# Kernel optimization log

Hardware: AMD Instinct MI355X
Metric: run time of the kernel (lower is better)

The kernel has to match this reference:

```python
import jax, jax.numpy as jnp
import numpy as np
from jax import lax

NPRE = 900        # num_proposal_pre (hardcoded in module)
NPOST = 64        # num_proposal init arg
MAXV = 8          # max vertices of intersection of two convex quads
NMS_THRESH = 0.85
BN_EPS = 1e-5


def boxes3d_to_bev(b):
    # b: (N,7) = (x,y,z,h,w,l,ry) -> BEV rotated box (x1,y1,x2,y2,ry) on x-z plane
    cu, cv = b[:, 0], b[:, 2]
    half_l, half_w = b[:, 5] * 0.5, b[:, 4] * 0.5
    return jnp.stack([cu - half_l, cv - half_w, cu + half_l, cv + half_w, b[:, 6]], axis=-1)


def rect_corners(bev):
    # bev: (N,5) -> (N,4,2) CCW corners of rotated rect
    cx = (bev[:, 0] + bev[:, 2]) * 0.5
    cy = (bev[:, 1] + bev[:, 3]) * 0.5
    hx = (bev[:, 2] - bev[:, 0]) * 0.5
    hy = (bev[:, 3] - bev[:, 1]) * 0.5
    c, s = jnp.cos(bev[:, 4]), jnp.sin(bev[:, 4])
    lx = jnp.stack([-hx, hx, hx, -hx], -1)   # (N,4)
    ly = jnp.stack([-hy, -hy, hy, hy], -1)
    X = cx[:, None] + c[:, None] * lx - s[:, None] * ly
    Y = cy[:, None] + s[:, None] * lx + c[:, None] * ly
    return jnp.stack([X, Y], -1)


def _clip(poly, cnt, a, b):
    # Sutherland-Hodgman clip of poly (MAXV,2) with cnt valid verts by half-plane
    # left of directed edge a->b (clip quad is CCW).
    n = b - a
    def side(p):
        return n[0] * (p[1] - a[1]) - n[1] * (p[0] - a[0])
    out = jnp.zeros_like(poly)
    ocnt = jnp.int32(0)
    for i in range(MAXV):
        valid = i < cnt
        cur = poly[i]
        nxt = poly[jnp.where(i + 1 < cnt, i + 1, 0)]
        dc, dn = side(cur), side(nxt)
        in_c, in_n = dc >= 0, dn >= 0
        e1 = valid & in_c
        out = jnp.where(e1, out.at[ocnt].set(cur), out)
        ocnt = ocnt + e1.astype(jnp.int32)
        e2 = valid & (in_c != in_n)
        denom = dc - dn
        t = dc / jnp.where(denom == 0, 1.0, denom)
        ip = cur + t * (nxt - cur)
        out = jnp.where(e2, out.at[ocnt].set(ip), out)
        ocnt = ocnt + e2.astype(jnp.int32)
    return out, ocnt


def _pair_inter(ca, cb):
    # intersection area of two convex quads given CCW corners (4,2)
    poly = jnp.concatenate([ca, jnp.zeros((MAXV - 4, 2), ca.dtype)], 0)
    cnt = jnp.int32(4)
    for k in range(4):
        poly, cnt = _clip(poly, cnt, cb[k], cb[(k + 1) % 4])
    s = jnp.float32(0.0)
    for i in range(MAXV):
        valid = (i < cnt) & (cnt >= 3)
        j = jnp.where(i + 1 < cnt, i + 1, 0)
        s = s + jnp.where(valid, poly[i, 0] * poly[j, 1] - poly[j, 0] * poly[i, 1], 0.0)
    return jnp.abs(s) * 0.5


def pairwise_iou(corners, areas):
    # row-blocked to keep memory small: lax.map over rows, vmap over cols
    def row(args):
        ci, ai = args
        inter = jax.vmap(lambda cj: _pair_inter(ci, cj))(corners)
        return inter / jnp.maximum(ai + areas - inter, 1e-8)
    return lax.map(row, (corners, areas))


def nms_keep(iou):
    N = iou.shape[0]
    idx = jnp.arange(N)
    def body(i, keep):
        sup = keep[i] & (iou[i] > NMS_THRESH) & (idx > i)
        return keep & (~sup)
    return lax.fori_loop(0, N, body, jnp.ones((N,), bool))


def _forward(search_xyz, search_feature, estimation_cla, template_box,
             W1, b1, gamma, beta, run_mean, run_var, W2, b2):
    B, N = search_xyz.shape[0], search_xyz.shape[1]
    # reg head: conv1d(256->128,k1) + BN(eval) + ReLU + dropout(eval=id) + conv1d(128->4,k1)
    h = jnp.einsum('oi,bin->bon', W1, search_feature) + b1[None, :, None]
    inv = gamma / jnp.sqrt(run_var + BN_EPS)
    h = h * inv[None, :, None] + (beta - run_mean * inv)[None, :, None]
    h = jax.nn.relu(h)
    offset = jnp.einsum('oi,bin->bon', W2, h) + b2[None, :, None]  # (B,4,N)
    offset = jnp.transpose(offset, (0, 2, 1))                       # (B,N,4)
    vote_xyz = search_xyz + offset[..., 0:3]
    tmpl = jnp.broadcast_to(template_box, (B, N, 7))
    proposals = jnp.concatenate([vote_xyz, tmpl[..., 3:6], offset[..., 3:4]], -1)  # (B,N,7)
    scores = jax.nn.sigmoid(estimation_cla[..., 0])  # (B,N)

    def per_batch(sc, pr):
        order = jnp.argsort(-sc)
        s = sc[order[:NPRE]]
        p = pr[order[:NPRE]]
        bev = boxes3d_to_bev(p)
        corners = rect_corners(bev)
        areas = (bev[:, 2] - bev[:, 0]) * (bev[:, 3] - bev[:, 1])
        iou = pairwise_iou(lax.stop_gradient(corners), lax.stop_gradient(areas))
        keep = nms_keep(iou)
        rank = jnp.cumsum(keep.astype(jnp.int32)) - 1
        tgt = jnp.where(keep & (rank < NPOST), rank, NPOST)  # NPOST = dummy slot
        out_b = jnp.zeros((NPOST + 1, 7), p.dtype).at[tgt].set(p)[:NPOST]
        out_s = jnp.zeros((NPOST + 1,), s.dtype).at[tgt].set(s)[:NPOST]
        return out_b, out_s

    ret_bbox3d, ret_scores = jax.vmap(per_batch)(scores, proposals)
    center_xyzs = ret_bbox3d[..., 0:3]
    prop_out = jnp.take(proposals, jnp.array([0, 1, 2, 6]), axis=-1)
    return ret_bbox3d, ret_scores, prop_out, center_xyzs


def setup_inputs():
    key = jax.random.key(0)
    ks = jax.random.split(key, 8)
    B, N, C, H = 8, 16384, 256, 128
    search_xyz = jax.random.normal(ks[0], (B, N, 3), jnp.float32) * 2.0
    search_feature = jax.random.normal(ks[1], (B, C, N), jnp.float32)
    estimation_cla = jax.random.normal(ks[2], (B, N, 1), jnp.float32)
    center = jax.random.normal(ks[3], (B, 1, 3), jnp.float32)
    dims = jax.random.uniform(ks[4], (B, 1, 3), jnp.float32, 1.0, 3.0)
    ry = jax.random.uniform(ks[5], (B, 1, 1), jnp.float32, -np.pi, np.pi)
    template_box = jnp.concatenate([center, dims, ry], -1)
    W1 = jax.random.normal(ks[6], (H, C), jnp.float32) * (1.0 / np.sqrt(C))
    b1 = jnp.zeros((H,), jnp.float32)
    gamma = jnp.ones((H,), jnp.float32)
    beta = jnp.zeros((H,), jnp.float32)
    run_mean = jnp.zeros((H,), jnp.float32)
    run_var = jnp.ones((H,), jnp.float32)
    W2 = jax.random.normal(ks[7], (4, H), jnp.float32) * (1.0 / np.sqrt(H))
    b2 = jnp.zeros((4,), jnp.float32)
    return dict(search_xyz=search_xyz, search_feature=search_feature,
                estimation_cla=estimation_cla, template_box=template_box,
                W1=W1, b1=b1, gamma=gamma, beta=beta,
                run_mean=run_mean, run_var=run_var, W2=W2, b2=b2)


def reference(search_xyz, search_feature, estimation_cla, template_box,
              W1, b1, gamma, beta, run_mean, run_var, W2, b2):
    return _forward(search_xyz, search_feature, estimation_cla, template_box,
                    W1, b1, gamma, beta, run_mean, run_var, W2, b2)
```

## Files before the change

### kernel.cpp

```cpp
#include <hip/hip_runtime.h>
#include <cmath>

#define NTOT 16384
#define NBATCH 8
#define NPRE 900
#define NPOST 64

__global__ __launch_bounds__(256) void mlp_kernel(
    const float* __restrict__ feat, const float* __restrict__ xyz,
    const float* __restrict__ W1, const float* __restrict__ b1,
    const float* __restrict__ gamma, const float* __restrict__ beta,
    const float* __restrict__ rmean, const float* __restrict__ rvar,
    const float* __restrict__ W2, const float* __restrict__ b2,
    float* __restrict__ prop) {
  __shared__ float As[64][128];
  __shared__ float Bs[64][128];
  const int b  = blockIdx.y;
  const int n0 = blockIdx.x * 128;
  const int tid = threadIdx.x;
  const int tr = tid >> 4, tc = tid & 15;
  const float* fb = feat + (size_t)b * 256 * NTOT;

  float acc[8][8];
#pragma unroll
  for (int r = 0; r < 8; ++r)
#pragma unroll
    for (int c = 0; c < 8; ++c) acc[r][c] = 0.f;

  for (int kt = 0; kt < 4; ++kt) {
    {
      const int m = tid & 127, qh = tid >> 7;
#pragma unroll
      for (int p = 0; p < 8; ++p) {
        const int q = qh + p * 2;
        const float4 w = *(const float4*)(W1 + (size_t)m * 256 + kt * 64 + q * 4);
        As[q * 4 + 0][m] = w.x; As[q * 4 + 1][m] = w.y;
        As[q * 4 + 2][m] = w.z; As[q * 4 + 3][m] = w.w;
      }
      const int qq = tid & 31, r0 = tid >> 5;
#pragma unroll
      for (int p = 0; p < 8; ++p) {
        const int k = r0 + p * 8;
        *(float4*)(&Bs[k][qq * 4]) =
            *(const float4*)(fb + (size_t)(kt * 64 + k) * NTOT + n0 + qq * 4);
      }
    }
    __syncthreads();
#pragma unroll 8
    for (int k = 0; k < 64; ++k) {
      float a[8], bb[8];
      *(float4*)&a[0]  = *(const float4*)&As[k][tr * 8];
      *(float4*)&a[4]  = *(const float4*)&As[k][tr * 8 + 4];
      *(float4*)&bb[0] = *(const float4*)&Bs[k][tc * 4];
      *(float4*)&bb[4] = *(const float4*)&Bs[k][64 + tc * 4];
#pragma unroll
      for (int r = 0; r < 8; ++r)
#pragma unroll
        for (int c = 0; c < 8; ++c) acc[r][c] = fmaf(a[r], bb[c], acc[r][c]);
    }
    __syncthreads();
  }

  float po[4][8];
#pragma unroll
  for (int kk = 0; kk < 4; ++kk)
#pragma unroll
    for (int c = 0; c < 8; ++c) po[kk][c] = 0.f;
#pragma unroll
  for (int r = 0; r < 8; ++r) {
    const int row = tr * 8 + r;
    const float inv = gamma[row] / sqrtf(rvar[row] + 1e-5f);
    const float sh  = beta[row] - rmean[row] * inv;
    const float bb1 = b1[row];
    float w2v[4];
#pragma unroll
    for (int kk = 0; kk < 4; ++kk) w2v[kk] = W2[kk * 128 + row];
#pragma unroll
    for (int c = 0; c < 8; ++c) {
      float h = (acc[r][c] + bb1) * inv + sh;
      h = fmaxf(h, 0.f);
#pragma unroll
      for (int kk = 0; kk < 4; ++kk) po[kk][c] += w2v[kk] * h;
    }
  }
  float* po_lds = &As[0][0];
#pragma unroll
  for (int kk = 0; kk < 4; ++kk)
#pragma unroll
    for (int c = 0; c < 8; ++c) {
      const int col = (c < 4) ? (tc * 4 + c) : (64 + tc * 4 + (c - 4));
      po_lds[((tr * 4 + kk) * 128) + col] = po[kk][c];
    }
  __syncthreads();
  float* off_lds = &Bs[0][0];
#pragma unroll
  for (int it = 0; it < 2; ++it) {
    const int idx = tid + it * 256;
    const int kk = idx >> 7, col = idx & 127;
    float sum = b2[kk];
#pragma unroll
    for (int t2 = 0; t2 < 16; ++t2) sum += po_lds[((t2 * 4 + kk) * 128) + col];
    off_lds[kk * 128 + col] = sum;
  }
  __syncthreads();
  if (tid < 128) {
    const int n = n0 + tid;
    const float* sx = xyz + ((size_t)b * NTOT + n) * 3;
    float4 o;
    o.x = sx[0] + off_lds[0 * 128 + tid];
    o.y = sx[1] + off_lds[1 * 128 + tid];
    o.z = sx[2] + off_lds[2 * 128 + tid];
    o.w = off_lds[3 * 128 + tid];
    *(float4*)(prop + ((size_t)b * NTOT + n) * 4) = o;
  }
}

__global__ __launch_bounds__(1024) void select_kernel(
    const float* __restrict__ cla, const float* __restrict__ prop,
    const float* __restrict__ tmpl, float* __restrict__ selbox,
    float* __restrict__ corners, float* __restrict__ areas,
    float* __restrict__ aabb) {
  __shared__ unsigned red[17];
  __shared__ int cnt_lds;
  __shared__ unsigned long long cand[1024];
  const int b = blockIdx.x, tid = threadIdx.x;
  unsigned key[16];
#pragma unroll
  for (int q = 0; q < 16; ++q) {
    const float x = cla[(size_t)b * NTOT + q * 1024 + tid];
    key[q] = __float_as_uint(1.0f / (1.0f + expf(-x)));
  }
  unsigned lo = 0u, hi = 0xFFFFFFFFu;
  while (hi - lo > 1u) {
    const unsigned mid = lo + ((hi - lo) >> 1);
    int c = 0;
#pragma unroll
    for (int q = 0; q < 16; ++q) c += (key[q] >= mid) ? 1 : 0;
#pragma unroll
    for (int off = 32; off > 0; off >>= 1) c += __shfl_down(c, off);
    __syncthreads();
    if ((tid & 63) == 0) red[tid >> 6] = (unsigned)c;
    __syncthreads();
    if (tid == 0) {
      unsigned s = 0;
      for (int w2 = 0; w2 < 16; ++w2) s += red[w2];
      red[16] = s;
    }
    __syncthreads();
    if (red[16] >= NPRE) lo = mid; else hi = mid;
  }
  const unsigned T = lo;
  if (tid == 0) cnt_lds = 0;
  cand[tid] = 0ull;
  __syncthreads();
#pragma unroll
  for (int q = 0; q < 16; ++q) {
    if (key[q] >= T) {
      const int pos = atomicAdd(&cnt_lds, 1);
      if (pos < 1024)
        cand[pos] = ((unsigned long long)key[q] << 32) |
                    (unsigned long long)(0xFFFFFFFFu - (unsigned)(q * 1024 + tid));
    }
  }
  __syncthreads();
  for (int k = 2; k <= 1024; k <<= 1) {
    for (int j = k >> 1; j > 0; j >>= 1) {
      if (tid < 512) {
        const int i = ((tid & ~(j - 1)) << 1) | (tid & (j - 1));
        const int l = i | j;
        const unsigned long long Pi = cand[i], Pl = cand[l];
        const bool asc = (i & k) == 0;
        if ((Pi < Pl) == asc) { cand[i] = Pl; cand[l] = Pi; }
      }
      __syncthreads();
    }
  }
  if (tid < NPRE) {
    const unsigned long long p = cand[tid];
    const int idx = (int)(0xFFFFFFFFu - (unsigned)(p & 0xFFFFFFFFull));
    const float score = __uint_as_float((unsigned)(p >> 32));
    const float4 pv = *(const float4*)(prop + ((size_t)b * NTOT + idx) * 4);
    const float d3 = tmpl[b * 7 + 3], d4 = tmpl[b * 7 + 4], d5 = tmpl[b * 7 + 5];
    const size_t o8 = ((size_t)b * NPRE + tid) * 8;
    selbox[o8 + 0] = pv.x; selbox[o8 + 1] = pv.y; selbox[o8 + 2] = pv.z;
    selbox[o8 + 3] = d3;   selbox[o8 + 4] = d4;   selbox[o8 + 5] = d5;
    selbox[o8 + 6] = pv.w; selbox[o8 + 7] = score;
    {
#pragma clang fp contract(off)
      const float cu = pv.x, cv = pv.z;
      const float hl = d5 * 0.5f, hw = d4 * 0.5f;
      const float x1 = cu - hl, y1 = cv - hw, x2 = cu + hl, y2 = cv + hw;
      const float cx = (x1 + x2) * 0.5f, cy = (y1 + y2) * 0.5f;
      const float hx = (x2 - x1) * 0.5f, hy = (y2 - y1) * 0.5f;
      const float cr = cosf(pv.w), sr = sinf(pv.w);
      const float lx[4] = {-hx, hx, hx, -hx};
      const float ly[4] = {-hy, -hy, hy, hy};
      float bx0 = 1e30f, by0 = 1e30f, bx1 = -1e30f, by1 = -1e30f;
#pragma unroll
      for (int q = 0; q < 4; ++q) {
        const float X = cx + cr * lx[q] - sr * ly[q];
        const float Y = cy + sr * lx[q] + cr * ly[q];
        corners[o8 + 2 * q]     = X;
        corners[o8 + 2 * q + 1] = Y;
        bx0 = fminf(bx0, X); by0 = fminf(by0, Y);
        bx1 = fmaxf(bx1, X); by1 = fmaxf(by1, Y);
      }
      areas[(size_t)b * NPRE + tid] = (x2 - x1) * (y2 - y1);
      float4 bb; bb.x = bx0; bb.y = by0; bb.z = bx1; bb.w = by1;
      *(float4*)(aabb + ((size_t)b * NPRE + tid) * 4) = bb;
    }
  }
}

__device__ __forceinline__ float polyclip_reg(
    float s0x, float s0y, float s1x, float s1y,
    float s2x, float s2y, float s3x, float s3y,
    const float cjx[4], const float cjy[4]) {
#pragma clang fp contract(off)
  float vx[8], vy[8];
  vx[0] = s0x; vy[0] = s0y; vx[1] = s1x; vy[1] = s1y;
  vx[2] = s2x; vy[2] = s2y; vx[3] = s3x; vy[3] = s3y;
#pragma unroll
  for (int v = 4; v < 8; ++v) { vx[v] = 0.f; vy[v] = 0.f; }
  int cnt = 4;
#pragma unroll
  for (int e = 0; e < 4; ++e) {
    const float ax = cjx[e], ay = cjy[e];
    const float bx = cjx[(e + 1) & 3], by = cjy[(e + 1) & 3];
    const float nx = bx - ax, ny = by - ay;
    float d[8];
#pragma unroll
    for (int v = 0; v < 8; ++v) d[v] = nx * (vy[v] - ay) - ny * (vx[v] - ax);
    float ox[8], oy[8];
#pragma unroll
    for (int v = 0; v < 8; ++v) { ox[v] = 0.f; oy[v] = 0.f; }
    int oc = 0;
#pragma unroll
    for (int v = 0; v < 8; ++v) {
      const bool valid = v < cnt;
      float nvx, nvy, dn;
      if (v == 7) {
        const bool big = cnt > 8;
        nvx = big ? vx[7] : vx[0]; nvy = big ? vy[7] : vy[0]; dn = big ? d[7] : d[0];
      } else {
        const bool wrap = (v + 1 >= cnt);
        nvx = wrap ? vx[0] : vx[v + 1];
        nvy = wrap ? vy[0] : vy[v + 1];
        dn  = wrap ? d[0]  : d[v + 1];
      }
      const float dc = d[v];
      const bool inc = dc >= 0.f, inn = dn >= 0.f;
      const bool e1 = valid && inc;
#pragma unroll
      for (int s2 = 0; s2 < 8; ++s2) {
        const bool w_ = e1 && (oc == s2);
        ox[s2] = w_ ? vx[v] : ox[s2];
        oy[s2] = w_ ? vy[v] : oy[s2];
      }
      oc += e1 ? 1 : 0;
      const bool e2 = valid && (inc != inn);
      const float den = dc - dn;
      const float t = dc / ((den == 0.f) ? 1.0f : den);
      const float ipx = vx[v] + t * (nvx - vx[v]);
      const float ipy = vy[v] + t * (nvy - vy[v]);
#pragma unroll
      for (int s2 = 0; s2 < 8; ++s2) {
        const bool w_ = e2 && (oc == s2);
        ox[s2] = w_ ? ipx : ox[s2];
        oy[s2] = w_ ? ipy : oy[s2];
      }
      oc += e2 ? 1 : 0;
    }
#pragma unroll
    for (int v = 0; v < 8; ++v) { vx[v] = ox[v]; vy[v] = oy[v]; }
    cnt = oc;
  }
  float s = 0.f;
#pragma unroll
  for (int v = 0; v < 8; ++v) {
    const bool valid = (v < cnt) && (cnt >= 3);
    float jx, jy;
    if (v == 7) {
      const bool big = cnt > 8;
      jx = big ? vx[7] : vx[0]; jy = big ? vy[7] : vy[0];
    } else {
      const bool wrap = (v + 1 >= cnt);
      jx = wrap ? vx[0] : vx[v + 1]; jy = wrap ? vy[0] : vy[v + 1];
    }
    s += valid ? (vx[v] * jy - jx * vy[v]) : 0.f;
  }
  return fabsf(s) * 0.5f;
}

__global__ __launch_bounds__(256) void iou_kernel(
    const float* __restrict__ corners, const float* __restrict__ areas,
    const float* __restrict__ aabb, unsigned long long* __restrict__ sup) {
  const int i = blockIdx.x, b = blockIdx.y, tid = threadIdx.x;
  const float* ci = corners + ((size_t)b * NPRE + i) * 8;
  const float ai = areas[(size_t)b * NPRE + i];
  const float4 bi = *(const float4*)(aabb + ((size_t)b * NPRE + i) * 4);
  const float s0x = ci[0], s0y = ci[1], s1x = ci[2], s1y = ci[3];
  const float s2x = ci[4], s2y = ci[5], s3x = ci[6], s3y = ci[7];
  for (int c = 0; c < 4; ++c) {
    const int j = c * 256 + tid;
    bool bit = false;
    if (j > i && j < NPRE) {
      const float4 bj = *(const float4*)(aabb + ((size_t)b * NPRE + j) * 4);
      const float aj = areas[(size_t)b * NPRE + j];
      const float ow = fminf(bi.z, bj.z) - fmaxf(bi.x, bj.x);
      const float oh = fminf(bi.w, bj.w) - fmaxf(bi.y, bj.y);
      const float ov = fmaxf(ow, 0.f) * fmaxf(oh, 0.f);
      if (ov >= 0.45f * (ai + aj)) {
        const float* cj = corners + ((size_t)b * NPRE + j) * 8;
        float cjx[4], cjy[4];
#pragma unroll
        for (int q = 0; q < 4; ++q) { cjx[q] = cj[2 * q]; cjy[q] = cj[2 * q + 1]; }
        const float inter = polyclip_reg(s0x, s0y, s1x, s1y, s2x, s2y,
                                         s3x, s3y, cjx, cjy);
        const float iou = inter / fmaxf(ai + aj - inter, 1e-8f);
        bit = iou > 0.85f;
      }
    }
    const unsigned long long m = __ballot(bit);
    if ((tid & 63) == 0)
      sup[((size_t)b * NPRE + i) * 16 + (unsigned)(j >> 6)] = m;
  }
}

#define NMS_ROWS 904
__global__ __launch_bounds__(1024) void nms_kernel(
    const unsigned long long* __restrict__ sup,
    unsigned long long* __restrict__ keepw) {
  extern __shared__ unsigned long long rows[];
  const int b = blockIdx.x, tid = threadIdx.x;
  const unsigned long long* srow = sup + (size_t)b * NPRE * 16;
  for (int q = tid; q < NMS_ROWS * 16; q += 1024)
    rows[q] = (q < NPRE * 16) ? srow[q] : 0ull;
  __syncthreads();
  if (tid < 64) {
    const int lane = tid;
    const bool ld = lane < 16;
    unsigned long long kw = 0ull;
    if (lane < 14) kw = ~0ull;
    else if (lane == 14) kw = 0xFull;
    unsigned long long r0 = ld ? rows[0 * 16 + lane] : 0ull;
    unsigned long long r1 = ld ? rows[1 * 16 + lane] : 0ull;
    unsigned long long r2 = ld ? rows[2 * 16 + lane] : 0ull;
    unsigned long long r3 = ld ? rows[3 * 16 + lane] : 0ull;
#define NMS_STEP(ii, bufv)                                            \
    {                                                                 \
      const unsigned long long w = __shfl(kw, (ii) >> 6);             \
      if ((w >> ((ii) & 63)) & 1ull) kw &= ~(bufv);                   \
      bufv = ld ? rows[((ii) + 4) * 16 + lane] : 0ull;                \
    }
    for (int i = 0; i < NPRE; i += 4) {
      NMS_STEP(i + 0, r0)
      NMS_STEP(i + 1, r1)
      NMS_STEP(i + 2, r2)
      NMS_STEP(i + 3, r3)
    }
#undef NMS_STEP
    if (lane < 15) keepw[b * 16 + lane] = kw;
  }
}

__global__ __launch_bounds__(128) void out_kernel(
    const float* __restrict__ selbox,
    const unsigned long long* __restrict__ keepw, float* __restrict__ out) {
  const int b = blockIdx.x, t = threadIdx.x;
  float* retb = out + (size_t)b * (NPOST * 7);
  float* rets = out + (size_t)NBATCH * NPOST * 7 + (size_t)b * NPOST;
  float* cent = out + (size_t)NBATCH * NPOST * 7 + (size_t)NBATCH * NPOST +
                (size_t)NBATCH * NTOT * 4 + (size_t)b * (NPOST * 3);
  for (int q = t; q < NPOST * 7; q += 128) retb[q] = 0.f;
  if (t < NPOST) rets[t] = 0.f;
  for (int q = t; q < NPOST * 3; q += 128) cent[q] = 0.f;
  __syncthreads();
  if (t < 64) {
    const unsigned long long kws = (t < 15) ? keepw[b * 16 + t] : 0ull;
    const int pc = __popcll(kws);
    int inc = pc;
    for (int d2 = 1; d2 < 64; d2 <<= 1) {
      const int up = __shfl_up(inc, d2);
      if (t >= d2) inc += up;
    }
    const int ex = inc - pc;
    for (int it = 0; it < 15; ++it) {
      const int i = t + it * 64;
      const int w = (i >> 6) & 63;
      const unsigned long long kword = __shfl(kws, w);
      const int exw = __shfl(ex, w);
      if (i < NPRE) {
        const int bp = i & 63;
        if ((kword >> bp) & 1ull) {
          const int rank =
              exw + __popcll(kword & (((unsigned long long)1 << bp) - 1ull));
          if (rank < NPOST) {
            const float* sb = selbox + ((size_t)b * NPRE + i) * 8;
#pragma unroll
            for (int c = 0; c < 7; ++c) retb[rank * 7 + c] = sb[c];
            rets[rank] = sb[7];
            cent[rank * 3 + 0] = sb[0];
            cent[rank * 3 + 1] = sb[1];
            cent[rank * 3 + 2] = sb[2];
          }
        }
      }
    }
  }
}

extern "C" void kernel_launch(void* const* d_in, const int* in_sizes, int n_in,
                              void* d_out, int out_size, void* d_ws, size_t ws_size,
                              hipStream_t stream) {
  const float* xyz   = (const float*)d_in[0];
  const float* feat  = (const float*)d_in[1];
  const float* cla   = (const float*)d_in[2];
  const float* tmpl  = (const float*)d_in[3];
  const float* W1    = (const float*)d_in[4];
  const float* b1    = (const float*)d_in[5];
  const float* gamma = (const float*)d_in[6];
  const float* beta  = (const float*)d_in[7];
  const float* rmean = (const float*)d_in[8];
  const float* rvar  = (const float*)d_in[9];
  const float* W2    = (const float*)d_in[10];
  const float* b2    = (const float*)d_in[11];
  float* out  = (float*)d_out;
  float* prop = out + (size_t)NBATCH * NPOST * 7 + (size_t)NBATCH * NPOST;

  char* ws = (char*)d_ws;
  float* selbox  = (float*)(ws);
  float* corners = (float*)(ws + 230400);
  float* areas   = (float*)(ws + 460800);
  float* aabb    = (float*)(ws + 489600);
  unsigned long long* sup   = (unsigned long long*)(ws + 604800);
  unsigned long long* keepw = (unsigned long long*)(ws + 1526400);

  mlp_kernel<<<dim3(NTOT / 128, NBATCH), 256, 0, stream>>>(
      feat, xyz, W1, b1, gamma, beta, rmean, rvar, W2, b2, prop);

  select_kernel<<<NBATCH, 1024, 0, stream>>>(cla, prop, tmpl, selbox, corners,
                                             areas, aabb);

  iou_kernel<<<dim3(NPRE, NBATCH), 256, 0, stream>>>(corners, areas, aabb, sup);

  (void)hipFuncSetAttribute((const void*)nms_kernel,
                            hipFuncAttributeMaxDynamicSharedMemorySize,
                            NMS_ROWS * 16 * (int)sizeof(unsigned long long));
  nms_kernel<<<NBATCH, 1024, NMS_ROWS * 16 * sizeof(unsigned long long),
               stream>>>(sup, keepw);

  out_kernel<<<NBATCH, 128, 0, stream>>>(selbox, keepw, out);
}
```

Before: 526.1 us.

## Compact AABB-passing pairs into worklist before polygon clipping; early-exit threshold search

```diff
diff --git a/kernel.cpp b/kernel.cpp
--- a/kernel.cpp
+++ b/kernel.cpp
@@ -115,15 +115,112 @@
   }
 }
 
+__device__ __forceinline__ float polyclip_reg(
+    float s0x, float s0y, float s1x, float s1y,
+    float s2x, float s2y, float s3x, float s3y,
+    const float cjx[4], const float cjy[4]) {
+#pragma clang fp contract(off)
+  float vx[8], vy[8];
+  vx[0] = s0x; vy[0] = s0y; vx[1] = s1x; vy[1] = s1y;
+  vx[2] = s2x; vy[2] = s2y; vx[3] = s3x; vy[3] = s3y;
+#pragma unroll
+  for (int v = 4; v < 8; ++v) { vx[v] = 0.f; vy[v] = 0.f; }
+  int cnt = 4;
+#pragma unroll
+  for (int e = 0; e < 4; ++e) {
+    const float ax = cjx[e], ay = cjy[e];
+    const float bx = cjx[(e + 1) & 3], by = cjy[(e + 1) & 3];
+    const float nx = bx - ax, ny = by - ay;
+    float d[8];
+#pragma unroll
+    for (int v = 0; v < 8; ++v) d[v] = nx * (vy[v] - ay) - ny * (vx[v] - ax);
+    float ox[8], oy[8];
+#pragma unroll
+    for (int v = 0; v < 8; ++v) { ox[v] = 0.f; oy[v] = 0.f; }
+    int oc = 0;
+#pragma unroll
+    for (int v = 0; v < 8; ++v) {
+      const bool valid = v < cnt;
+      float nvx, nvy, dn;
+      if (v == 7) {
+        const bool big = cnt > 8;
+        nvx = big ? vx[7] : vx[0]; nvy = big ? vy[7] : vy[0]; dn = big ? d[7] : d[0];
+      } else {
+        const bool wrap = (v + 1 >= cnt);
+        nvx = wrap ? vx[0] : vx[v + 1];
+        nvy = wrap ? vy[0] : vy[v + 1];
+        dn  = wrap ? d[0]  : d[v + 1];
+      }
+      const float dc = d[v];
+      const bool inc = dc >= 0.f, inn = dn >= 0.f;
+      const bool e1 = valid && inc;
+#pragma unroll
+      for (int s2 = 0; s2 < 8; ++s2) {
+        const bool w_ = e1 && (oc == s2);
+        ox[s2] = w_ ? vx[v] : ox[s2];
+        oy[s2] = w_ ? vy[v] : oy[s2];
+      }
+      oc += e1 ? 1 : 0;
+      const bool e2 = valid && (inc != inn);
+      const float den = dc - dn;
+      const float t = dc / ((den == 0.f) ? 1.0f : den);
+      const float ipx = vx[v] + t * (nvx - vx[v]);
+      const float ipy = vy[v] + t * (nvy - vy[v]);
+#pragma unroll
+      for (int s2 = 0; s2 < 8; ++s2) {
+        const bool w_ = e2 && (oc == s2);
+        ox[s2] = w_ ? ipx : ox[s2];
+        oy[s2] = w_ ? ipy : oy[s2];
+      }
+      oc += e2 ? 1 : 0;
+    }
+#pragma unroll
+    for (int v = 0; v < 8; ++v) { vx[v] = ox[v]; vy[v] = oy[v]; }
+    cnt = oc;
+  }
+  float s = 0.f;
+#pragma unroll
+  for (int v = 0; v < 8; ++v) {
+    const bool valid = (v < cnt) && (cnt >= 3);
+    float jx, jy;
+    if (v == 7) {
+      const bool big = cnt > 8;
+      jx = big ? vx[7] : vx[0]; jy = big ? vy[7] : vy[0];
+    } else {
+      const bool wrap = (v + 1 >= cnt);
+      jx = wrap ? vx[0] : vx[v + 1]; jy = wrap ? vy[0] : vy[v + 1];
+    }
+    s += valid ? (vx[v] * jy - jx * vy[v]) : 0.f;
+  }
+  return fabsf(s) * 0.5f;
+}
+
+__device__ __forceinline__ bool pair_suppressed(
+    const float* __restrict__ corners, const float* __restrict__ areas,
+    int b, int i, int j) {
+  const float* ci = corners + ((size_t)b * NPRE + i) * 8;
+  const float* cj = corners + ((size_t)b * NPRE + j) * 8;
+  float cjx[4], cjy[4];
+#pragma unroll
+  for (int q = 0; q < 4; ++q) { cjx[q] = cj[2 * q]; cjy[q] = cj[2 * q + 1]; }
+  const float inter = polyclip_reg(ci[0], ci[1], ci[2], ci[3],
+                                   ci[4], ci[5], ci[6], ci[7], cjx, cjy);
+  const float ai = areas[(size_t)b * NPRE + i];
+  const float aj = areas[(size_t)b * NPRE + j];
+  const float iou = inter / fmaxf(ai + aj - inter, 1e-8f);
+  return iou > 0.85f;
+}
+
 __global__ __launch_bounds__(1024) void select_kernel(
     const float* __restrict__ cla, const float* __restrict__ prop,
     const float* __restrict__ tmpl, float* __restrict__ selbox,
     float* __restrict__ corners, float* __restrict__ areas,
-    float* __restrict__ aabb) {
+    float* __restrict__ aabb, int* __restrict__ wlcnt) {
   __shared__ unsigned red[17];
   __shared__ int cnt_lds;
   __shared__ unsigned long long cand[1024];
   const int b = blockIdx.x, tid = threadIdx.x;
+  if (tid == 0) wlcnt[b] = 0;
   unsigned key[16];
 #pragma unroll
   for (int q = 0; q < 16; ++q) {
@@ -131,7 +228,9 @@
     key[q] = __float_as_uint(1.0f / (1.0f + expf(-x)));
   }
   unsigned lo = 0u, hi = 0xFFFFFFFFu;
-  while (hi - lo > 1u) {
+  unsigned T = 0u;
+  bool done = false;
+  while (!done && (hi - lo > 1u)) {
     const unsigned mid = lo + ((hi - lo) >> 1);
     int c = 0;
 #pragma unroll
@@ -147,9 +246,12 @@
       red[16] = s;
     }
     __syncthreads();
-    if (red[16] >= NPRE) lo = mid; else hi = mid;
-  }
-  const unsigned T = lo;
+    const unsigned cntv = red[16];
+    if (cntv >= NPRE && cntv <= 1024) { T = mid; done = true; }
+    else if (cntv >= NPRE) lo = mid;
+    else hi = mid;
+  }
+  if (!done) T = lo;
   if (tid == 0) cnt_lds = 0;
   cand[tid] = 0ull;
   __syncthreads();
@@ -212,118 +314,78 @@
   }
 }
 
-__device__ __forceinline__ float polyclip_reg(
-    float s0x, float s0y, float s1x, float s1y,
-    float s2x, float s2y, float s3x, float s3y,
-    const float cjx[4], const float cjy[4]) {
-#pragma clang fp contract(off)
-  float vx[8], vy[8];
-  vx[0] = s0x; vy[0] = s0y; vx[1] = s1x; vy[1] = s1y;
-  vx[2] = s2x; vy[2] = s2y; vx[3] = s3x; vy[3] = s3y;
-#pragma unroll
-  for (int v = 4; v < 8; ++v) { vx[v] = 0.f; vy[v] = 0.f; }
-  int cnt = 4;
-#pragma unroll
-  for (int e = 0; e < 4; ++e) {
-    const float ax = cjx[e], ay = cjy[e];
-    const float bx = cjx[(e + 1) & 3], by = cjy[(e + 1) & 3];
-    const float nx = bx - ax, ny = by - ay;
-    float d[8];
-#pragma unroll
-    for (int v = 0; v < 8; ++v) d[v] = nx * (vy[v] - ay) - ny * (vx[v] - ax);
-    float ox[8], oy[8];
-#pragma unroll
-    for (int v = 0; v < 8; ++v) { ox[v] = 0.f; oy[v] = 0.f; }
-    int oc = 0;
-#pragma unroll
-    for (int v = 0; v < 8; ++v) {
-      const bool valid = v < cnt;
-      float nvx, nvy, dn;
-      if (v == 7) {
-        const bool big = cnt > 8;
-        nvx = big ? vx[7] : vx[0]; nvy = big ? vy[7] : vy[0]; dn = big ? d[7] : d[0];
-      } else {
-        const bool wrap = (v + 1 >= cnt);
-        nvx = wrap ? vx[0] : vx[v + 1];
-        nvy = wrap ? vy[0] : vy[v + 1];
-        dn  = wrap ? d[0]  : d[v + 1];
-      }
-      const float dc = d[v];
-      const bool inc = dc >= 0.f, inn = dn >= 0.f;
-      const bool e1 = valid && inc;
-#pragma unroll
-      for (int s2 = 0; s2 < 8; ++s2) {
-        const bool w_ = e1 && (oc == s2);
-        ox[s2] = w_ ? vx[v] : ox[s2];
-        oy[s2] = w_ ? vy[v] : oy[s2];
-      }
-      oc += e1 ? 1 : 0;
-      const bool e2 = valid && (inc != inn);
-      const float den = dc - dn;
-      const float t = dc / ((den == 0.f) ? 1.0f : den);
-      const float ipx = vx[v] + t * (nvx - vx[v]);
-      const float ipy = vy[v] + t * (nvy - vy[v]);
-#pragma unroll
-      for (int s2 = 0; s2 < 8; ++s2) {
-        const bool w_ = e2 && (oc == s2);
-        ox[s2] = w_ ? ipx : ox[s2];
-        oy[s2] = w_ ? ipy : oy[s2];
-      }
-      oc += e2 ? 1 : 0;
-    }
-#pragma unroll
-    for (int v = 0; v < 8; ++v) { vx[v] = ox[v]; vy[v] = oy[v]; }
-    cnt = oc;
-  }
-  float s = 0.f;
-#pragma unroll
-  for (int v = 0; v < 8; ++v) {
-    const bool valid = (v < cnt) && (cnt >= 3);
-    float jx, jy;
-    if (v == 7) {
-      const bool big = cnt > 8;
-      jx = big ? vx[7] : vx[0]; jy = big ? vy[7] : vy[0];
-    } else {
-      const bool wrap = (v + 1 >= cnt);
-      jx = wrap ? vx[0] : vx[v + 1]; jy = wrap ? vy[0] : vy[v + 1];
-    }
-    s += valid ? (vx[v] * jy - jx * vy[v]) : 0.f;
-  }
-  return fabsf(s) * 0.5f;
-}
-
-__global__ __launch_bounds__(256) void iou_kernel(
-    const float* __restrict__ corners, const float* __restrict__ areas,
-    const float* __restrict__ aabb, unsigned long long* __restrict__ sup) {
+__global__ __launch_bounds__(256) void pairgen_kernel(
+    const float* __restrict__ aabb, const float* __restrict__ areas,
+    const float* __restrict__ corners, unsigned long long* __restrict__ sup,
+    unsigned* __restrict__ wl, int* __restrict__ wlcnt, int cap) {
+  __shared__ int wsum[4];
+  __shared__ int base_s;
   const int i = blockIdx.x, b = blockIdx.y, tid = threadIdx.x;
-  const float* ci = corners + ((size_t)b * NPRE + i) * 8;
+  if (tid < 16) sup[((size_t)b * NPRE + i) * 16 + tid] = 0ull;
+  const float4 bi = *(const float4*)(aabb + ((size_t)b * NPRE + i) * 4);
   const float ai = areas[(size_t)b * NPRE + i];
-  const float4 bi = *(const float4*)(aabb + ((size_t)b * NPRE + i) * 4);
-  const float s0x = ci[0], s0y = ci[1], s1x = ci[2], s1y = ci[3];
-  const float s2x = ci[4], s2y = ci[5], s3x = ci[6], s3y = ci[7];
+  bool pass[4];
+  int pc = 0;
+#pragma unroll
   for (int c = 0; c < 4; ++c) {
     const int j = c * 256 + tid;
-    bool bit = false;
+    bool p = false;
     if (j > i && j < NPRE) {
       const float4 bj = *(const float4*)(aabb + ((size_t)b * NPRE + j) * 4);
       const float aj = areas[(size_t)b * NPRE + j];
       const float ow = fminf(bi.z, bj.z) - fmaxf(bi.x, bj.x);
       const float oh = fminf(bi.w, bj.w) - fmaxf(bi.y, bj.y);
       const float ov = fmaxf(ow, 0.f) * fmaxf(oh, 0.f);
-      if (ov >= 0.45f * (ai + aj)) {
-        const float* cj = corners + ((size_t)b * NPRE + j) * 8;
-        float cjx[4], cjy[4];
-#pragma unroll
-        for (int q = 0; q < 4; ++q) { cjx[q] = cj[2 * q]; cjy[q] = cj[2 * q + 1]; }
-        const float inter = polyclip_reg(s0x, s0y, s1x, s1y, s2x, s2y,
-                                         s3x, s3y, cjx, cjy);
-        const float iou = inter / fmaxf(ai + aj - inter, 1e-8f);
-        bit = iou > 0.85f;
-      }
-    }
-    const unsigned long long m = __ballot(bit);
-    if ((tid & 63) == 0)
-      sup[((size_t)b * NPRE + i) * 16 + (unsigned)(j >> 6)] = m;
+      p = (ov >= 0.45f * (ai + aj));
+    }
+    pass[c] = p;
+    pc += p ? 1 : 0;
+  }
+  int inc = pc;
+#pragma unroll
+  for (int d2 = 1; d2 < 64; d2 <<= 1) {
+    const int u = __shfl_up(inc, d2);
+    if ((tid & 63) >= d2) inc += u;
+  }
+  if ((tid & 63) == 63) wsum[tid >> 6] = inc;
+  __syncthreads();
+  if (tid == 0) {
+    const int tot = wsum[0] + wsum[1] + wsum[2] + wsum[3];
+    base_s = (tot > 0) ? atomicAdd(&wlcnt[b], tot) : 0;
+  }
+  __syncthreads();
+  int wbase = 0;
+#pragma unroll
+  for (int w = 0; w < 4; ++w)
+    if (w < (tid >> 6)) wbase += wsum[w];
+  int myoff = base_s + wbase + (inc - pc);
+#pragma unroll
+  for (int c = 0; c < 4; ++c) {
+    if (pass[c]) {
+      const int j = c * 256 + tid;
+      const int pos = myoff++;
+      if (pos < cap) {
+        wl[(size_t)b * cap + pos] = (unsigned)((i << 10) | j);
+      } else {
+        if (pair_suppressed(corners, areas, b, i, j))
+          atomicOr(&sup[((size_t)b * NPRE + i) * 16 + (j >> 6)],
+                   1ull << (j & 63));
+      }
+    }
+  }
+}
+
+__global__ __launch_bounds__(256) void clip_kernel(
+    const float* __restrict__ corners, const float* __restrict__ areas,
+    const unsigned* __restrict__ wl, const int* __restrict__ wlcnt, int cap,
+    unsigned long long* __restrict__ sup) {
+  const int b = blockIdx.y, tid = threadIdx.x;
+  const int n = min(wlcnt[b], cap);
+  for (int idx = blockIdx.x * 256 + tid; idx < n; idx += gridDim.x * 256) {
+    const unsigned e = wl[(size_t)b * cap + idx];
+    const int i = (int)(e >> 10), j = (int)(e & 1023u);
+    if (pair_suppressed(corners, areas, b, i, j))
+      atomicOr(&sup[((size_t)b * NPRE + i) * 16 + (j >> 6)], 1ull << (j & 63));
   }
 }
 
@@ -435,14 +497,24 @@
   float* aabb    = (float*)(ws + 489600);
   unsigned long long* sup   = (unsigned long long*)(ws + 604800);
   unsigned long long* keepw = (unsigned long long*)(ws + 1526400);
+  int* wlcnt = (int*)(ws + 1527424);
+  unsigned* wl = (unsigned*)(ws + 1527456);
+  long long avail = (long long)ws_size - 1527456;
+  if (avail < 0) avail = 0;
+  int cap = (int)(avail / (4 * NBATCH));
+  if (cap > 404551) cap = 404551;
 
   mlp_kernel<<<dim3(NTOT / 128, NBATCH), 256, 0, stream>>>(
       feat, xyz, W1, b1, gamma, beta, rmean, rvar, W2, b2, prop);
 
   select_kernel<<<NBATCH, 1024, 0, stream>>>(cla, prop, tmpl, selbox, corners,
-                                             areas, aabb);
-
-  iou_kernel<<<dim3(NPRE, NBATCH), 256, 0, stream>>>(corners, areas, aabb, sup);
+                                             areas, aabb, wlcnt);
+
+  pairgen_kernel<<<dim3(NPRE, NBATCH), 256, 0, stream>>>(
+      aabb, areas, corners, sup, wl, wlcnt, cap);
+
+  clip_kernel<<<dim3(64, NBATCH), 256, 0, stream>>>(corners, areas, wl, wlcnt,
+                                                    cap, sup);
 
   (void)hipFuncSetAttribute((const void*)nms_kernel,
                             hipFuncAttributeMaxDynamicSharedMemorySize,
```

Measured after the change: 477.2 us. -9.3%, faster.
